# Kernel optimization log

Measured on AMD Instinct MI355X. Metric: run time of the kernel, lower is better.

Reference implementation:

```python
import jax, jax.numpy as jnp
import numpy as np


def setup_inputs() -> dict:
    key = jax.random.key(0)
    k1, k2 = jax.random.split(key)
    B, S, N_IN, RANK = 4, 1024, 1024, 64
    x = jax.random.normal(k1, (B, S, N_IN), dtype=jnp.float32)
    # nn.init.uniform_(projector, -0.05, 0.05)
    projector = jax.random.uniform(k2, (N_IN, RANK), dtype=jnp.float32,
                                   minval=-0.05, maxval=0.05)
    return {"x": x, "projector": projector}


def reference(x, projector):
    # x: [B, S, n_in], projector: [n_in, rank]
    t = jnp.matmul(x, projector)                      # [B, S, r]
    # pairwise squared distances: sum_r (t[b,i,r] - t[b,j,r])^2
    diffs = t[:, :, None, :] - t[:, None, :, :]       # [B, S, S, r]
    return jnp.sum(diffs * diffs, axis=-1)            # [B, S, S]
```

## Files before the change

kernel.cpp:

```cpp
#include <hip/hip_runtime.h>
#include <hip/hip_bf16.h>

typedef __attribute__((ext_vector_type(8))) short bf8_t;
typedef __attribute__((ext_vector_type(4))) float f4_t;

static __device__ __forceinline__ short f2bf(float f) {
    union { float f; unsigned u; } v; v.f = f;
    unsigned r = v.u + 0x7fffu + ((v.u >> 16) & 1u);
    return (short)(r >> 16);
}
static __device__ __forceinline__ float bf2f(short s) {
    union { unsigned u; float f; } v;
    v.u = ((unsigned)(unsigned short)s) << 16;
    return v.f;
}

__global__ void __launch_bounds__(256)
transpose_p(const float* __restrict__ P, short* __restrict__ Pt) {
    int idx = blockIdx.x * 256 + threadIdx.x;
    int n = idx >> 10, k = idx & 1023;
    Pt[idx] = f2bf(P[k * 64 + n]);
}

__global__ void __launch_bounds__(256)
proj_kernel(const float* __restrict__ x, const short* __restrict__ Pt,
            short* __restrict__ t, float* __restrict__ norms) {
    const int w    = threadIdx.x >> 6;
    const int lane = threadIdx.x & 63;
    const int nr   = lane & 15;
    const int quad = lane >> 4;
    const int row  = blockIdx.x * 16 + nr;

    f4_t acc[4];
    #pragma unroll
    for (int mt = 0; mt < 4; mt++) acc[mt] = f4_t{0.f, 0.f, 0.f, 0.f};

    const float* xr = x + (size_t)row * 1024;
    #pragma unroll
    for (int kt = 0; kt < 8; kt++) {
        const int kb = w * 256 + kt * 32 + quad * 8;
        f4_t x0 = *(const f4_t*)(xr + kb);
        f4_t x1 = *(const f4_t*)(xr + kb + 4);
        bf8_t bfr;
        bfr[0] = f2bf(x0[0]); bfr[1] = f2bf(x0[1]);
        bfr[2] = f2bf(x0[2]); bfr[3] = f2bf(x0[3]);
        bfr[4] = f2bf(x1[0]); bfr[5] = f2bf(x1[1]);
        bfr[6] = f2bf(x1[2]); bfr[7] = f2bf(x1[3]);
        #pragma unroll
        for (int mt = 0; mt < 4; mt++) {
            bf8_t afr = *(const bf8_t*)(Pt + (size_t)(mt * 16 + nr) * 1024 + kb);
            acc[mt] = __builtin_amdgcn_mfma_f32_16x16x32_bf16(afr, bfr, acc[mt], 0, 0, 0);
        }
    }

    __shared__ float red[3][16][64];
    if (w > 0) {
        #pragma unroll
        for (int mt = 0; mt < 4; mt++)
            #pragma unroll
            for (int r = 0; r < 4; r++)
                red[w - 1][mt * 4 + r][lane] = acc[mt][r];
    }
    __syncthreads();

    if (w == 0) {
        float nrm = 0.f;
        #pragma unroll
        for (int mt = 0; mt < 4; mt++) {
            float v0 = acc[mt][0] + red[0][mt*4+0][lane] + red[1][mt*4+0][lane] + red[2][mt*4+0][lane];
            float v1 = acc[mt][1] + red[0][mt*4+1][lane] + red[1][mt*4+1][lane] + red[2][mt*4+1][lane];
            float v2 = acc[mt][2] + red[0][mt*4+2][lane] + red[1][mt*4+2][lane] + red[2][mt*4+2][lane];
            float v3 = acc[mt][3] + red[0][mt*4+3][lane] + red[1][mt*4+3][lane] + red[2][mt*4+3][lane];
            short s0 = f2bf(v0), s1 = f2bf(v1), s2 = f2bf(v2), s3 = f2bf(v3);
            float b0 = bf2f(s0), b1 = bf2f(s1), b2 = bf2f(s2), b3 = bf2f(s3);
            nrm += b0*b0 + b1*b1 + b2*b2 + b3*b3;
            short4 sv; sv.x = s0; sv.y = s1; sv.z = s2; sv.w = s3;
            *(short4*)(t + (size_t)row * 64 + mt * 16 + quad * 4) = sv;
        }
        nrm += __shfl_xor(nrm, 16);
        nrm += __shfl_xor(nrm, 32);
        if (quad == 0) norms[row] = nrm;
    }
}

__global__ void __launch_bounds__(256)
pairwise_kernel(const short* __restrict__ t, const float* __restrict__ norms,
                float* __restrict__ out) {
    const int b    = blockIdx.y;
    const int ti   = blockIdx.x >> 3;
    const int tj   = blockIdx.x & 7;
    const int w    = threadIdx.x >> 6;
    const int lane = threadIdx.x & 63;
    const int wy   = w >> 1, wx = w & 1;
    const int i0   = ti * 128 + wy * 64;
    const int j0   = tj * 128 + wx * 64;
    const int nr   = lane & 15, quad = lane >> 4;

    __shared__ float ni[128], nj[128];
    if (threadIdx.x < 128) ni[threadIdx.x]       = norms[b * 1024 + ti * 128 + threadIdx.x];
    else                   nj[threadIdx.x - 128] = norms[b * 1024 + tj * 128 + (threadIdx.x - 128)];
    __syncthreads();

    const short* tb = t + (size_t)b * 1024 * 64;

    f4_t acc[4][4];
    #pragma unroll
    for (int ia = 0; ia < 4; ia++)
        #pragma unroll
        for (int jb = 0; jb < 4; jb++) acc[ia][jb] = f4_t{0.f, 0.f, 0.f, 0.f};

    #pragma unroll
    for (int kt = 0; kt < 2; kt++) {
        const int kb = kt * 32 + quad * 8;
        bf8_t A[4], B[4];
        #pragma unroll
        for (int ia = 0; ia < 4; ia++)
            A[ia] = *(const bf8_t*)(tb + (size_t)(i0 + ia * 16 + nr) * 64 + kb);
        #pragma unroll
        for (int jb = 0; jb < 4; jb++)
            B[jb] = *(const bf8_t*)(tb + (size_t)(j0 + jb * 16 + nr) * 64 + kb);
        #pragma unroll
        for (int ia = 0; ia < 4; ia++)
            #pragma unroll
            for (int jb = 0; jb < 4; jb++)
                acc[ia][jb] = __builtin_amdgcn_mfma_f32_16x16x32_bf16(A[ia], B[jb], acc[ia][jb], 0, 0, 0);
    }

    #pragma unroll
    for (int ia = 0; ia < 4; ia++) {
        #pragma unroll
        for (int r = 0; r < 4; r++) {
            const int irow = i0 + ia * 16 + quad * 4 + r;
            const float niv = ni[wy * 64 + ia * 16 + quad * 4 + r];
            float* orow = out + ((size_t)b * 1024 + irow) * 1024 + j0 + nr;
            #pragma unroll
            for (int jb = 0; jb < 4; jb++) {
                float v = niv + nj[wx * 64 + jb * 16 + nr] - 2.f * acc[ia][jb][r];
                orow[jb * 16] = v;
            }
        }
    }
}

extern "C" void kernel_launch(void* const* d_in, const int* in_sizes, int n_in,
                              void* d_out, int out_size, void* d_ws, size_t ws_size,
                              hipStream_t stream) {
    const float* x = (const float*)d_in[0];
    const float* P = (const float*)d_in[1];
    float* out = (float*)d_out;

    short* Pt    = (short*)d_ws;
    short* t     = (short*)d_ws + 65536;
    float* norms = (float*)((char*)d_ws + (128 + 512) * 1024);

    transpose_p<<<256, 256, 0, stream>>>(P, Pt);
    proj_kernel<<<256, 256, 0, stream>>>(x, Pt, t, norms);
    dim3 g2(64, 4);
    pairwise_kernel<<<g2, 256, 0, stream>>>(t, norms, out);
}
```

Baseline: 79.78 us.

## Fuse three kernels into one persistent kernel with grid barriers and vectorized stores

Merges the projector transpose, projection and pairwise-distance kernels into a single 256-block launch separated by atomic-counter grid barriers, with a memset to reset the counters. This removes two kernel launch gaps. The pairwise stage also swaps the MFMA operands so each lane holds four consecutive output columns, allowing float4 stores instead of scalar strided stores. The risks are spin-wait barrier latency, an extra memset launch, and deadlock if not all 256 blocks are co-resident.

```diff
diff --git a/kernel.cpp b/kernel.cpp
--- a/kernel.cpp
+++ b/kernel.cpp
@@ -1,5 +1,4 @@
 #include <hip/hip_runtime.h>
-#include <hip/hip_bf16.h>
 
 typedef __attribute__((ext_vector_type(8))) short bf8_t;
 typedef __attribute__((ext_vector_type(4))) float f4_t;
@@ -15,128 +14,154 @@
     return v.f;
 }
 
-__global__ void __launch_bounds__(256)
-transpose_p(const float* __restrict__ P, short* __restrict__ Pt) {
-    int idx = blockIdx.x * 256 + threadIdx.x;
-    int n = idx >> 10, k = idx & 1023;
-    Pt[idx] = f2bf(P[k * 64 + n]);
+#define NBLK 256u
+
+static __device__ __forceinline__ void grid_barrier(unsigned* cnt) {
+    __syncthreads();
+    if (threadIdx.x == 0) {
+        __hip_atomic_fetch_add(cnt, 1u, __ATOMIC_RELEASE, __HIP_MEMORY_SCOPE_AGENT);
+        while (__hip_atomic_load(cnt, __ATOMIC_ACQUIRE, __HIP_MEMORY_SCOPE_AGENT) < NBLK) {
+            __builtin_amdgcn_s_sleep(1);
+        }
+        __threadfence();
+    }
+    __syncthreads();
 }
 
-__global__ void __launch_bounds__(256)
-proj_kernel(const float* __restrict__ x, const short* __restrict__ Pt,
-            short* __restrict__ t, float* __restrict__ norms) {
-    const int w    = threadIdx.x >> 6;
-    const int lane = threadIdx.x & 63;
-    const int nr   = lane & 15;
-    const int quad = lane >> 4;
-    const int row  = blockIdx.x * 16 + nr;
+__global__ void __launch_bounds__(256, 2)
+fused(const float* __restrict__ x, const float* __restrict__ P,
+      float* __restrict__ out, short* __restrict__ Pt,
+      short* __restrict__ t, float* __restrict__ norms,
+      unsigned* __restrict__ bar)
+{
+    const int tid = threadIdx.x;
+    const int bid = blockIdx.x;
 
-    f4_t acc[4];
-    #pragma unroll
-    for (int mt = 0; mt < 4; mt++) acc[mt] = f4_t{0.f, 0.f, 0.f, 0.f};
+    __shared__ float red[3][16][64];
+    __shared__ float ni[128], nj[128];
 
-    const float* xr = x + (size_t)row * 1024;
-    #pragma unroll
-    for (int kt = 0; kt < 8; kt++) {
-        const int kb = w * 256 + kt * 32 + quad * 8;
-        f4_t x0 = *(const f4_t*)(xr + kb);
-        f4_t x1 = *(const f4_t*)(xr + kb + 4);
-        bf8_t bfr;
-        bfr[0] = f2bf(x0[0]); bfr[1] = f2bf(x0[1]);
-        bfr[2] = f2bf(x0[2]); bfr[3] = f2bf(x0[3]);
-        bfr[4] = f2bf(x1[0]); bfr[5] = f2bf(x1[1]);
-        bfr[6] = f2bf(x1[2]); bfr[7] = f2bf(x1[3]);
+    {
+        int idx = bid * 256 + tid;
+        int n = idx >> 10, k = idx & 1023;
+        Pt[idx] = f2bf(P[k * 64 + n]);
+    }
+    grid_barrier(bar + 0);
+
+    {
+        const int w    = tid >> 6;
+        const int lane = tid & 63;
+        const int nr   = lane & 15;
+        const int quad = lane >> 4;
+        const int row  = bid * 16 + nr;
+
+        f4_t acc[4];
         #pragma unroll
-        for (int mt = 0; mt < 4; mt++) {
-            bf8_t afr = *(const bf8_t*)(Pt + (size_t)(mt * 16 + nr) * 1024 + kb);
-            acc[mt] = __builtin_amdgcn_mfma_f32_16x16x32_bf16(afr, bfr, acc[mt], 0, 0, 0);
+        for (int mt = 0; mt < 4; mt++) acc[mt] = f4_t{0.f, 0.f, 0.f, 0.f};
+
+        const float* xr = x + (size_t)row * 1024;
+        #pragma unroll
+        for (int kt = 0; kt < 8; kt++) {
+            const int kb = w * 256 + kt * 32 + quad * 8;
+            f4_t x0 = *(const f4_t*)(xr + kb);
+            f4_t x1 = *(const f4_t*)(xr + kb + 4);
+            bf8_t bfr;
+            bfr[0] = f2bf(x0[0]); bfr[1] = f2bf(x0[1]);
+            bfr[2] = f2bf(x0[2]); bfr[3] = f2bf(x0[3]);
+            bfr[4] = f2bf(x1[0]); bfr[5] = f2bf(x1[1]);
+            bfr[6] = f2bf(x1[2]); bfr[7] = f2bf(x1[3]);
+            #pragma unroll
+            for (int mt = 0; mt < 4; mt++) {
+                bf8_t afr = *(const bf8_t*)(Pt + (size_t)(mt * 16 + nr) * 1024 + kb);
+                acc[mt] = __builtin_amdgcn_mfma_f32_16x16x32_bf16(afr, bfr, acc[mt], 0, 0, 0);
+            }
+        }
+
+        if (w > 0) {
+            #pragma unroll
+            for (int mt = 0; mt < 4; mt++)
+                #pragma unroll
+                for (int r = 0; r < 4; r++)
+                    red[w - 1][mt * 4 + r][lane] = acc[mt][r];
+        }
+        __syncthreads();
+
+        if (w == 0) {
+            float nrm = 0.f;
+            #pragma unroll
+            for (int mt = 0; mt < 4; mt++) {
+                float v0 = acc[mt][0] + red[0][mt*4+0][lane] + red[1][mt*4+0][lane] + red[2][mt*4+0][lane];
+                float v1 = acc[mt][1] + red[0][mt*4+1][lane] + red[1][mt*4+1][lane] + red[2][mt*4+1][lane];
+                float v2 = acc[mt][2] + red[0][mt*4+2][lane] + red[1][mt*4+2][lane] + red[2][mt*4+2][lane];
+                float v3 = acc[mt][3] + red[0][mt*4+3][lane] + red[1][mt*4+3][lane] + red[2][mt*4+3][lane];
+                short s0 = f2bf(v0), s1 = f2bf(v1), s2 = f2bf(v2), s3 = f2bf(v3);
+                float b0 = bf2f(s0), b1 = bf2f(s1), b2 = bf2f(s2), b3 = bf2f(s3);
+                nrm += b0*b0 + b1*b1 + b2*b2 + b3*b3;
+                short4 sv; sv.x = s0; sv.y = s1; sv.z = s2; sv.w = s3;
+                *(short4*)(t + (size_t)row * 64 + mt * 16 + quad * 4) = sv;
+            }
+            nrm += __shfl_xor(nrm, 16);
+            nrm += __shfl_xor(nrm, 32);
+            if (quad == 0) norms[row] = nrm;
         }
     }
+    grid_barrier(bar + 32);
 
-    __shared__ float red[3][16][64];
-    if (w > 0) {
-        #pragma unroll
-        for (int mt = 0; mt < 4; mt++)
-            #pragma unroll
-            for (int r = 0; r < 4; r++)
-                red[w - 1][mt * 4 + r][lane] = acc[mt][r];
-    }
-    __syncthreads();
+    {
+        const int b    = bid >> 6;
+        const int ti   = (bid >> 3) & 7;
+        const int tj   = bid & 7;
+        const int w    = tid >> 6;
+        const int lane = tid & 63;
+        const int wy   = w >> 1, wx = w & 1;
+        const int i0   = ti * 128 + wy * 64;
+        const int j0   = tj * 128 + wx * 64;
+        const int nr   = lane & 15, quad = lane >> 4;
 
-    if (w == 0) {
-        float nrm = 0.f;
-        #pragma unroll
-        for (int mt = 0; mt < 4; mt++) {
-            float v0 = acc[mt][0] + red[0][mt*4+0][lane] + red[1][mt*4+0][lane] + red[2][mt*4+0][lane];
-            float v1 = acc[mt][1] + red[0][mt*4+1][lane] + red[1][mt*4+1][lane] + red[2][mt*4+1][lane];
-            float v2 = acc[mt][2] + red[0][mt*4+2][lane] + red[1][mt*4+2][lane] + red[2][mt*4+2][lane];
-            float v3 = acc[mt][3] + red[0][mt*4+3][lane] + red[1][mt*4+3][lane] + red[2][mt*4+3][lane];
-            short s0 = f2bf(v0), s1 = f2bf(v1), s2 = f2bf(v2), s3 = f2bf(v3);
-            float b0 = bf2f(s0), b1 = bf2f(s1), b2 = bf2f(s2), b3 = bf2f(s3);
-            nrm += b0*b0 + b1*b1 + b2*b2 + b3*b3;
-            short4 sv; sv.x = s0; sv.y = s1; sv.z = s2; sv.w = s3;
-            *(short4*)(t + (size_t)row * 64 + mt * 16 + quad * 4) = sv;
-        }
-        nrm += __shfl_xor(nrm, 16);
-        nrm += __shfl_xor(nrm, 32);
-        if (quad == 0) norms[row] = nrm;
-    }
-}
+        if (tid < 128) ni[tid]       = norms[b * 1024 + ti * 128 + tid];
+        else           nj[tid - 128] = norms[b * 1024 + tj * 128 + (tid - 128)];
+        __syncthreads();
 
-__global__ void __launch_bounds__(256)
-pairwise_kernel(const short* __restrict__ t, const float* __restrict__ norms,
-                float* __restrict__ out) {
-    const int b    = blockIdx.y;
-    const int ti   = blockIdx.x >> 3;
-    const int tj   = blockIdx.x & 7;
-    const int w    = threadIdx.x >> 6;
-    const int lane = threadIdx.x & 63;
-    const int wy   = w >> 1, wx = w & 1;
-    const int i0   = ti * 128 + wy * 64;
-    const int j0   = tj * 128 + wx * 64;
-    const int nr   = lane & 15, quad = lane >> 4;
+        const short* tb = t + (size_t)b * 1024 * 64;
 
-    __shared__ float ni[128], nj[128];
-    if (threadIdx.x < 128) ni[threadIdx.x]       = norms[b * 1024 + ti * 128 + threadIdx.x];
-    else                   nj[threadIdx.x - 128] = norms[b * 1024 + tj * 128 + (threadIdx.x - 128)];
-    __syncthreads();
-
-    const short* tb = t + (size_t)b * 1024 * 64;
-
-    f4_t acc[4][4];
-    #pragma unroll
-    for (int ia = 0; ia < 4; ia++)
-        #pragma unroll
-        for (int jb = 0; jb < 4; jb++) acc[ia][jb] = f4_t{0.f, 0.f, 0.f, 0.f};
-
-    #pragma unroll
-    for (int kt = 0; kt < 2; kt++) {
-        const int kb = kt * 32 + quad * 8;
-        bf8_t A[4], B[4];
-        #pragma unroll
-        for (int ia = 0; ia < 4; ia++)
-            A[ia] = *(const bf8_t*)(tb + (size_t)(i0 + ia * 16 + nr) * 64 + kb);
-        #pragma unroll
-        for (int jb = 0; jb < 4; jb++)
-            B[jb] = *(const bf8_t*)(tb + (size_t)(j0 + jb * 16 + nr) * 64 + kb);
+        f4_t acc[4][4];
         #pragma unroll
         for (int ia = 0; ia < 4; ia++)
             #pragma unroll
+            for (int jb = 0; jb < 4; jb++) acc[ia][jb] = f4_t{0.f, 0.f, 0.f, 0.f};
+
+        #pragma unroll
+        for (int kt = 0; kt < 2; kt++) {
+            const int kb = kt * 32 + quad * 8;
+            bf8_t A[4], B[4];
+            #pragma unroll
             for (int jb = 0; jb < 4; jb++)
-                acc[ia][jb] = __builtin_amdgcn_mfma_f32_16x16x32_bf16(A[ia], B[jb], acc[ia][jb], 0, 0, 0);
-    }
+                A[jb] = *(const bf8_t*)(tb + (size_t)(j0 + jb * 16 + nr) * 64 + kb);
+            #pragma unroll
+            for (int ia = 0; ia < 4; ia++)
+                B[ia] = *(const bf8_t*)(tb + (size_t)(i0 + ia * 16 + nr) * 64 + kb);
+            #pragma unroll
+            for (int ia = 0; ia < 4; ia++)
+                #pragma unroll
+                for (int jb = 0; jb < 4; jb++)
+                    acc[ia][jb] = __builtin_amdgcn_mfma_f32_16x16x32_bf16(A[jb], B[ia], acc[ia][jb], 0, 0, 0);
+        }
 
-    #pragma unroll
-    for (int ia = 0; ia < 4; ia++) {
         #pragma unroll
-        for (int r = 0; r < 4; r++) {
-            const int irow = i0 + ia * 16 + quad * 4 + r;
-            const float niv = ni[wy * 64 + ia * 16 + quad * 4 + r];
-            float* orow = out + ((size_t)b * 1024 + irow) * 1024 + j0 + nr;
+        for (int ia = 0; ia < 4; ia++) {
+            const int i = i0 + ia * 16 + nr;
+            const float niv = ni[wy * 64 + ia * 16 + nr];
+            float* orow = out + ((size_t)b * 1024 + i) * 1024 + tj * 128;
             #pragma unroll
             for (int jb = 0; jb < 4; jb++) {
-                float v = niv + nj[wx * 64 + jb * 16 + nr] - 2.f * acc[ia][jb][r];
-                orow[jb * 16] = v;
+                const int jo = wx * 64 + jb * 16 + quad * 4;
+                const float4 nv = *(const float4*)&nj[jo];
+                f4_t a = acc[ia][jb];
+                float4 v;
+                v.x = niv + nv.x - 2.f * a[0];
+                v.y = niv + nv.y - 2.f * a[1];
+                v.z = niv + nv.z - 2.f * a[2];
+                v.w = niv + nv.w - 2.f * a[3];
+                *(float4*)(orow + jo) = v;
             }
         }
     }
@@ -149,12 +174,11 @@
     const float* P = (const float*)d_in[1];
     float* out = (float*)d_out;
 
-    short* Pt    = (short*)d_ws;
-    short* t     = (short*)d_ws + 65536;
-    float* norms = (float*)((char*)d_ws + (128 + 512) * 1024);
+    short*    Pt    = (short*)d_ws;
+    short*    t     = (short*)d_ws + 65536;
+    float*    norms = (float*)((char*)d_ws + 640 * 1024);
+    unsigned* bar   = (unsigned*)((char*)d_ws + (1 << 20));
 
-    transpose_p<<<256, 256, 0, stream>>>(P, Pt);
-    proj_kernel<<<256, 256, 0, stream>>>(x, Pt, t, norms);
-    dim3 g2(64, 4);
-    pairwise_kernel<<<g2, 256, 0, stream>>>(t, norms, out);
+    hipMemsetAsync(bar, 0, 256, stream);
+    fused<<<256, 256, 0, stream>>>(x, P, out, Pt, t, norms, bar);
 }
```

Result: slower. 112.5 us (+41.0%).

## Shrink pairwise tiles, swap MFMA operands for float4 stores, swizzle blocks

Applied to the files above, without the earlier changes.

Pairwise tiles shrink from 128x128 to 64x64 per block, so the grid grows from 256 to 1024 blocks and there is more parallelism for the store-bound output. The MFMA operands are swapped so each lane holds four consecutive output columns, and the epilogue writes with float4 stores instead of scalar strided stores. A block-index swizzle remaps blocks across tiles, and launch bounds are raised to allow four blocks per CU. The trade is less reuse of the t operand per block in exchange for wider, better-coalesced writes and higher occupancy.

```diff
diff --git a/kernel.cpp b/kernel.cpp
--- a/kernel.cpp
+++ b/kernel.cpp
@@ -1,5 +1,4 @@
 #include <hip/hip_runtime.h>
-#include <hip/hip_bf16.h>
 
 typedef __attribute__((ext_vector_type(8))) short bf8_t;
 typedef __attribute__((ext_vector_type(4))) float f4_t;
@@ -83,61 +82,68 @@
     }
 }
 
-__global__ void __launch_bounds__(256)
+__global__ void __launch_bounds__(256, 4)
 pairwise_kernel(const short* __restrict__ t, const float* __restrict__ norms,
-                float* __restrict__ out) {
+                float* __restrict__ out)
+{
     const int b    = blockIdx.y;
-    const int ti   = blockIdx.x >> 3;
-    const int tj   = blockIdx.x & 7;
-    const int w    = threadIdx.x >> 6;
-    const int lane = threadIdx.x & 63;
+    const int swz  = (blockIdx.x & 7) * 32 + (blockIdx.x >> 3);
+    const int ti   = swz >> 4;
+    const int tj   = swz & 15;
+    const int tid  = threadIdx.x;
+    const int w    = tid >> 6;
+    const int lane = tid & 63;
     const int wy   = w >> 1, wx = w & 1;
-    const int i0   = ti * 128 + wy * 64;
-    const int j0   = tj * 128 + wx * 64;
+    const int i0   = ti * 64 + wy * 32;
+    const int j0   = tj * 64 + wx * 32;
     const int nr   = lane & 15, quad = lane >> 4;
 
-    __shared__ float ni[128], nj[128];
-    if (threadIdx.x < 128) ni[threadIdx.x]       = norms[b * 1024 + ti * 128 + threadIdx.x];
-    else                   nj[threadIdx.x - 128] = norms[b * 1024 + tj * 128 + (threadIdx.x - 128)];
+    __shared__ float ni[64], nj[64];
+    if (tid < 64)       ni[tid]      = norms[b * 1024 + ti * 64 + tid];
+    else if (tid < 128) nj[tid - 64] = norms[b * 1024 + tj * 64 + (tid - 64)];
     __syncthreads();
 
     const short* tb = t + (size_t)b * 1024 * 64;
 
-    f4_t acc[4][4];
+    f4_t acc[2][2];
     #pragma unroll
-    for (int ia = 0; ia < 4; ia++)
+    for (int ia = 0; ia < 2; ia++)
         #pragma unroll
-        for (int jb = 0; jb < 4; jb++) acc[ia][jb] = f4_t{0.f, 0.f, 0.f, 0.f};
+        for (int jb = 0; jb < 2; jb++) acc[ia][jb] = f4_t{0.f, 0.f, 0.f, 0.f};
 
     #pragma unroll
     for (int kt = 0; kt < 2; kt++) {
         const int kb = kt * 32 + quad * 8;
-        bf8_t A[4], B[4];
+        bf8_t A[2], B[2];
         #pragma unroll
-        for (int ia = 0; ia < 4; ia++)
-            A[ia] = *(const bf8_t*)(tb + (size_t)(i0 + ia * 16 + nr) * 64 + kb);
+        for (int jb = 0; jb < 2; jb++)
+            A[jb] = *(const bf8_t*)(tb + (size_t)(j0 + jb * 16 + nr) * 64 + kb);
         #pragma unroll
-        for (int jb = 0; jb < 4; jb++)
-            B[jb] = *(const bf8_t*)(tb + (size_t)(j0 + jb * 16 + nr) * 64 + kb);
+        for (int ia = 0; ia < 2; ia++)
+            B[ia] = *(const bf8_t*)(tb + (size_t)(i0 + ia * 16 + nr) * 64 + kb);
         #pragma unroll
-        for (int ia = 0; ia < 4; ia++)
+        for (int ia = 0; ia < 2; ia++)
             #pragma unroll
-            for (int jb = 0; jb < 4; jb++)
-                acc[ia][jb] = __builtin_amdgcn_mfma_f32_16x16x32_bf16(A[ia], B[jb], acc[ia][jb], 0, 0, 0);
+            for (int jb = 0; jb < 2; jb++)
+                acc[ia][jb] = __builtin_amdgcn_mfma_f32_16x16x32_bf16(A[jb], B[ia], acc[ia][jb], 0, 0, 0);
     }
 
     #pragma unroll
-    for (int ia = 0; ia < 4; ia++) {
+    for (int ia = 0; ia < 2; ia++) {
+        const int i = i0 + ia * 16 + nr;
+        const float niv = ni[wy * 32 + ia * 16 + nr];
+        float* orow = out + ((size_t)b * 1024 + i) * 1024 + tj * 64;
         #pragma unroll
-        for (int r = 0; r < 4; r++) {
-            const int irow = i0 + ia * 16 + quad * 4 + r;
-            const float niv = ni[wy * 64 + ia * 16 + quad * 4 + r];
-            float* orow = out + ((size_t)b * 1024 + irow) * 1024 + j0 + nr;
-            #pragma unroll
-            for (int jb = 0; jb < 4; jb++) {
-                float v = niv + nj[wx * 64 + jb * 16 + nr] - 2.f * acc[ia][jb][r];
-                orow[jb * 16] = v;
-            }
+        for (int jb = 0; jb < 2; jb++) {
+            const int jo = wx * 32 + jb * 16 + quad * 4;
+            const float4 nv = *(const float4*)&nj[jo];
+            f4_t a = acc[ia][jb];
+            float4 v;
+            v.x = niv + nv.x - 2.f * a[0];
+            v.y = niv + nv.y - 2.f * a[1];
+            v.z = niv + nv.z - 2.f * a[2];
+            v.w = niv + nv.w - 2.f * a[3];
+            *(float4*)(orow + jo) = v;
         }
     }
 }
@@ -155,6 +161,6 @@
 
     transpose_p<<<256, 256, 0, stream>>>(P, Pt);
     proj_kernel<<<256, 256, 0, stream>>>(x, Pt, t, norms);
-    dim3 g2(64, 4);
+    dim3 g2(256, 4);
     pairwise_kernel<<<g2, 256, 0, stream>>>(t, norms, out);
 }
```

Result: slower. 81.56 us (+2.2%).
